# Performance work log

Measured on AMD Instinct MI355X. Metric: run time of the kernel, lower is better.

## Reference

```python
import jax, jax.numpy as jnp
import numpy as np

NUM_HEADS = 12
DIM = 768
HEAD_DIM = DIM // NUM_HEADS


def setup_inputs() -> dict:
    key = jax.random.key(0)
    k1, k2, k3, k4 = jax.random.split(key, 4)
    B, N, C = 4, 8192, DIM
    x = jax.random.normal(k1, (B, N, C), dtype=jnp.float32)
    # torch nn.Linear stores weight as (out_features, in_features)
    W_qkv = jax.random.normal(k2, (3 * C, C), dtype=jnp.float32) * (1.0 / np.sqrt(C))
    W_proj = jax.random.normal(k3, (C, C), dtype=jnp.float32) * (1.0 / np.sqrt(C))
    b_proj = jax.random.normal(k4, (C,), dtype=jnp.float32) * 0.01
    return {"x": x, "W_qkv": W_qkv, "W_proj": W_proj, "b_proj": b_proj}


def reference(x, W_qkv, W_proj, b_proj):
    B, N, C = x.shape
    H, D = NUM_HEADS, HEAD_DIM
    qkv = x @ W_qkv.T                                  # [B,N,3C]
    qkv = qkv.reshape(B, N, 3, H, D).transpose(2, 0, 3, 1, 4)  # [3,B,H,N,D]
    q, k, v = qkv[0], qkv[1], qkv[2]
    q = jax.nn.elu(q) + 1.0
    k = jax.nn.elu(k) + 1.0
    k_sum = k.sum(axis=-2)                             # [B,H,D]
    kv = jnp.einsum('bhnd,bhne->bhde', k, v)           # [B,H,D,D]
    numerator = jnp.einsum('bhnd,bhde->bhne', q, kv)   # [B,H,N,D]
    denominator = jnp.einsum('bhnd,bhd->bhn', q, k_sum)
    out = numerator / (denominator[..., None] + 1e-6)
    out = out.transpose(0, 2, 1, 3).reshape(B, N, C)   # [B,N,C]
    out = out @ W_proj.T + b_proj
    return out
```

## Files before the change

kernel.cpp:

```cpp
#include <hip/hip_runtime.h>
#include <hip/hip_bf16.h>
#include <stdint.h>

typedef __attribute__((ext_vector_type(8))) short short8;
typedef __attribute__((ext_vector_type(4))) float floatx4;

#define NB 4
#define NN 8192
#define NC 768
#define NH 12
#define ND 64
#define LDQKV 2304
#define NSPLIT 16

__device__ __forceinline__ float bf2f(ushort u) {
    union { float f; uint32_t i; } x; x.i = ((uint32_t)u) << 16; return x.f;
}
__device__ __forceinline__ ushort f2bf(float f) {
    union { float f; uint32_t i; } x; x.f = f;
    uint32_t r = x.i + 0x7fff + ((x.i >> 16) & 1);
    return (ushort)(r >> 16);
}
typedef const __attribute__((address_space(1))) uint32_t* gas1_t;
typedef __attribute__((address_space(3))) uint32_t* las3_t;
__device__ __forceinline__ void gl_lds16(const void* g, const void* l) {
    __builtin_amdgcn_global_load_lds((gas1_t)(uintptr_t)g,
                                     (las3_t)(uint32_t)(uintptr_t)l, 16, 0, 0);
}

__global__ __launch_bounds__(256) void cvt_all(const float* __restrict__ X,
                                               const float* __restrict__ Wq,
                                               const float* __restrict__ Wp,
                                               ushort* __restrict__ xbf,
                                               ushort* __restrict__ wqbf,
                                               ushort* __restrict__ wpbf) {
    const int nx = 32768 * 768, nwq = 2304 * 768, nwp = 768 * 768;
    int i = (blockIdx.x * 256 + threadIdx.x) * 8;
    const float* src; ushort* dst;
    if (i < nx)            { src = X + i;              dst = xbf + i; }
    else if (i < nx + nwq) { i -= nx;  src = Wq + i;   dst = wqbf + i; }
    else                   { i -= nx + nwq; if (i >= nwp) return; src = Wp + i; dst = wpbf + i; }
    const float4 a = *(const float4*)src;
    const float4 b = *(const float4*)(src + 4);
    short8 v;
    v[0] = (short)f2bf(a.x); v[1] = (short)f2bf(a.y);
    v[2] = (short)f2bf(a.z); v[3] = (short)f2bf(a.w);
    v[4] = (short)f2bf(b.x); v[5] = (short)f2bf(b.y);
    v[6] = (short)f2bf(b.z); v[7] = (short)f2bf(b.w);
    *(short8*)dst = v;
}

template<int LDC, bool ELU, bool BIAS, typename OutT>
__global__ __launch_bounds__(256) void gemm_bt(const ushort* __restrict__ A,
                                               const ushort* __restrict__ Bw,
                                               const float* __restrict__ bias,
                                               OutT* __restrict__ Cout, int K) {
    __shared__ ushort As[2][128 * 32];
    __shared__ ushort Bs[2][128 * 32];
    const int t = threadIdx.x;
    const int w = t >> 6, lane = t & 63, l16 = lane & 15, quad = lane >> 4;
    const int wm = w & 1, wn = w >> 1;
    const int m0 = blockIdx.y * 128, n0 = blockIdx.x * 128;

    floatx4 acc[4][4] = {};

    const int rowA = t >> 2, chA = t & 3;
    const ushort* gA = A  + (size_t)(m0 + rowA) * K + chA * 8;
    const ushort* gB = Bw + (size_t)(n0 + rowA) * K + chA * 8;

    for (int k0 = 0; k0 < K; k0 += 64) {
        #pragma unroll
        for (int p = 0; p < 2; p++) {
            gl_lds16(gA + k0 + p * 32,                &As[p][w * 512]);
            gl_lds16(gA + k0 + p * 32 + 64 * (size_t)K, &As[p][2048 + w * 512]);
            gl_lds16(gB + k0 + p * 32,                &Bs[p][w * 512]);
            gl_lds16(gB + k0 + p * 32 + 64 * (size_t)K, &Bs[p][2048 + w * 512]);
        }
        __syncthreads();
        #pragma unroll
        for (int p = 0; p < 2; p++) {
            short8 af[4], bfr[4];
            #pragma unroll
            for (int i = 0; i < 4; i++)
                af[i] = *(const short8*)&As[p][(wm * 64 + i * 16 + l16) * 32 + quad * 8];
            #pragma unroll
            for (int j = 0; j < 4; j++)
                bfr[j] = *(const short8*)&Bs[p][(wn * 64 + j * 16 + l16) * 32 + quad * 8];
            #pragma unroll
            for (int i = 0; i < 4; i++)
                #pragma unroll
                for (int j = 0; j < 4; j++)
                    acc[i][j] = __builtin_amdgcn_mfma_f32_16x16x32_bf16(af[i], bfr[j], acc[i][j], 0, 0, 0);
        }
        __syncthreads();
    }

    #pragma unroll
    for (int i = 0; i < 4; i++) {
        const int row = m0 + wm * 64 + i * 16 + quad * 4;
        #pragma unroll
        for (int j = 0; j < 4; j++) {
            const int col = n0 + wn * 64 + j * 16 + l16;
            float bval = 0.f;
            if (BIAS) bval = bias[col];
            OutT* cp = Cout + (size_t)row * LDC + col;
            #pragma unroll
            for (int r = 0; r < 4; r++) {
                float v = acc[i][j][r];
                if (ELU) { if (col < 2 * NC) v = (v > 0.f) ? v + 1.f : __expf(v); }
                if (BIAS) v += bval;
                if (sizeof(OutT) == 2) *cp = (OutT)f2bf(v);
                else                   *cp = (OutT)v;
                cp += LDC;
            }
        }
    }
}

__global__ __launch_bounds__(256) void kv_ksum(const ushort* __restrict__ qkv,
                                               float* __restrict__ kvpart,
                                               float* __restrict__ kspart) {
    __shared__ ushort klds[128 * 64];
    __shared__ ushort vlds[128 * 64];
    __shared__ float  kvred[64 * 64];
    __shared__ float  ksred[4][64];
    const int bh = blockIdx.y, b = bh / NH, h = bh % NH;
    const int t = threadIdx.x, w = t >> 6, lane = t & 63, l16 = lane & 15, quad = lane >> 4;
    const int n0 = blockIdx.x * (NN * NB / NSPLIT / 4);
    const ushort* kbase = qkv + (size_t)(b * NN) * LDQKV + NC     + h * ND;
    const ushort* vbase = qkv + (size_t)(b * NN) * LDQKV + 2 * NC + h * ND;

    floatx4 acc[4][4] = {};
    floatx4 acc5[4] = {};
    short8 ones;
    #pragma unroll
    for (int j = 0; j < 8; j++) ones[j] = (l16 == 0) ? (short)0x3F80 : (short)0;

    const int rowT = t >> 3, ch = t & 7;

    for (int s = 0; s < 4; s++) {
        const int nb = n0 + s * 128;
        #pragma unroll
        for (int i = 0; i < 4; i++) {
            const size_t r = (size_t)(nb + i * 32 + rowT) * LDQKV + ch * 8;
            gl_lds16(kbase + r, klds + i * 2048 + w * 512);
            gl_lds16(vbase + r, vlds + i * 2048 + w * 512);
        }
        __syncthreads();
        short8 af[4], bfr[4];
        #pragma unroll
        for (int dt = 0; dt < 4; dt++) {
            short8 v;
            #pragma unroll
            for (int j = 0; j < 8; j++)
                v[j] = (short)klds[(w * 32 + quad * 8 + j) * 64 + dt * 16 + l16];
            af[dt] = v;
        }
        #pragma unroll
        for (int et = 0; et < 4; et++) {
            short8 v;
            #pragma unroll
            for (int j = 0; j < 8; j++)
                v[j] = (short)vlds[(w * 32 + quad * 8 + j) * 64 + et * 16 + l16];
            bfr[et] = v;
        }
        #pragma unroll
        for (int dt = 0; dt < 4; dt++) {
            #pragma unroll
            for (int et = 0; et < 4; et++)
                acc[dt][et] = __builtin_amdgcn_mfma_f32_16x16x32_bf16(af[dt], bfr[et], acc[dt][et], 0, 0, 0);
            acc5[dt] = __builtin_amdgcn_mfma_f32_16x16x32_bf16(af[dt], ones, acc5[dt], 0, 0, 0);
        }
        __syncthreads();
    }

    if (w == 0) {
        #pragma unroll
        for (int dt = 0; dt < 4; dt++)
            #pragma unroll
            for (int et = 0; et < 4; et++)
                #pragma unroll
                for (int r = 0; r < 4; r++)
                    kvred[(dt * 16 + quad * 4 + r) * 64 + et * 16 + l16] = acc[dt][et][r];
    }
    if (l16 == 0) {
        #pragma unroll
        for (int dt = 0; dt < 4; dt++)
            #pragma unroll
            for (int r = 0; r < 4; r++)
                ksred[w][dt * 16 + quad * 4 + r] = acc5[dt][r];
    }
    __syncthreads();
    if (w != 0) {
        #pragma unroll
        for (int dt = 0; dt < 4; dt++)
            #pragma unroll
            for (int et = 0; et < 4; et++)
                #pragma unroll
                for (int r = 0; r < 4; r++)
                    atomicAdd(&kvred[(dt * 16 + quad * 4 + r) * 64 + et * 16 + l16], acc[dt][et][r]);
    }
    __syncthreads();
    float* kvp = kvpart + ((size_t)blockIdx.x * 48 + bh) * 4096;
    for (int i = t; i < 4096; i += 256) kvp[i] = kvred[i];
    if (t < 64) kspart[((size_t)blockIdx.x * 48 + bh) * 64 + t] =
        ksred[0][t] + ksred[1][t] + ksred[2][t] + ksred[3][t];
}

__global__ __launch_bounds__(256) void reduce_kvks(const float* __restrict__ kvpart,
                                                   const float* __restrict__ kspart,
                                                   float* __restrict__ kvfinal,
                                                   float* __restrict__ ksfinal) {
    const int bh = blockIdx.y, t = threadIdx.x;
    if (blockIdx.x < 16) {
        const int i = blockIdx.x * 256 + t;
        float s = 0.f;
        #pragma unroll
        for (int p = 0; p < NSPLIT; p++) s += kvpart[((size_t)p * 48 + bh) * 4096 + i];
        kvfinal[(size_t)bh * 4096 + i] = s;
    } else if (t < 64) {
        float s = 0.f;
        #pragma unroll
        for (int p = 0; p < NSPLIT; p++) s += kspart[((size_t)p * 48 + bh) * 64 + t];
        ksfinal[bh * 64 + t] = s;
    }
}

__global__ __launch_bounds__(256) void attn_apply(const ushort* __restrict__ qkv,
                                                  const float* __restrict__ kvfinal,
                                                  const float* __restrict__ ksfinal,
                                                  ushort* __restrict__ outpre) {
    __shared__ ushort kvb[64 * 80];
    const int bh = blockIdx.y, b = bh / NH, h = bh % NH;
    const int t = threadIdx.x, w = t >> 6, lane = t & 63, l16 = lane & 15, quad = lane >> 4;

    for (int i = t; i < 4096; i += 256) {
        const int d = i >> 6, e = i & 63;
        kvb[d * 80 + e] = f2bf(kvfinal[(size_t)bh * 4096 + i]);
    }
    for (int i = t; i < 1024; i += 256) {
        const int d = i >> 4, c = i & 15;
        kvb[d * 80 + 64 + c] = (c == 0) ? f2bf(ksfinal[bh * 64 + d]) : (ushort)0;
    }
    __syncthreads();

    short8 bfr[5][2];
    #pragma unroll
    for (int et = 0; et < 5; et++)
        #pragma unroll
        for (int ks = 0; ks < 2; ks++) {
            short8 v;
            #pragma unroll
            for (int j = 0; j < 8; j++)
                v[j] = (short)kvb[(ks * 32 + quad * 8 + j) * 80 + et * 16 + l16];
            bfr[et][ks] = v;
        }

    const ushort* qbase = qkv + (size_t)(b * NN) * LDQKV + h * ND;
    ushort* obase = outpre + (size_t)(b * NN) * NC + h * ND;
    const int n0 = blockIdx.x * (NN * NB / NSPLIT / 4);

    for (int it = 0; it < 8; it++) {
        const int nt = n0 + (it * 4 + w) * 16;
        const ushort* qp = qbase + (size_t)(nt + l16) * LDQKV + quad * 8;
        const short8 a0 = *(const short8*)qp;
        const short8 a1 = *(const short8*)(qp + 32);
        floatx4 acc[5] = {};
        #pragma unroll
        for (int et = 0; et < 5; et++) {
            acc[et] = __builtin_amdgcn_mfma_f32_16x16x32_bf16(a0, bfr[et][0], acc[et], 0, 0, 0);
            acc[et] = __builtin_amdgcn_mfma_f32_16x16x32_bf16(a1, bfr[et][1], acc[et], 0, 0, 0);
        }
        float dv[4];
        #pragma unroll
        for (int r = 0; r < 4; r++) dv[r] = __shfl(acc[4][r], lane & 48);
        #pragma unroll
        for (int et = 0; et < 4; et++)
            #pragma unroll
            for (int r = 0; r < 4; r++) {
                const float o = acc[et][r] / (dv[r] + 1e-6f);
                obase[(size_t)(nt + quad * 4 + r) * NC + et * 16 + l16] = f2bf(o);
            }
    }
}

extern "C" void kernel_launch(void* const* d_in, const int* in_sizes, int n_in,
                              void* d_out, int out_size, void* d_ws, size_t ws_size,
                              hipStream_t stream) {
    (void)in_sizes; (void)n_in; (void)out_size; (void)ws_size;
    const float* X     = (const float*)d_in[0];
    const float* Wqkv  = (const float*)d_in[1];
    const float* Wproj = (const float*)d_in[2];
    const float* bproj = (const float*)d_in[3];
    float* out = (float*)d_out;

    char* ws = (char*)d_ws;
    size_t off = 0;
    ushort* qkv     = (ushort*)(ws + off); off += (size_t)32768 * 2304 * 2;
    ushort* outpre  = (ushort*)(ws + off); off += (size_t)32768 * 768 * 2;
    ushort* xbf     = (ushort*)(ws + off); off += (size_t)32768 * 768 * 2;
    ushort* wqkvbf  = (ushort*)(ws + off); off += (size_t)2304 * 768 * 2;
    ushort* wprojbf = (ushort*)(ws + off); off += (size_t)768 * 768 * 2;
    float* kvpart  = (float*)xbf;
    float* kspart  = kvpart + (size_t)NSPLIT * 48 * 4096;
    float* kvfinal = kspart + (size_t)NSPLIT * 48 * 64;
    float* ksfinal = kvfinal + (size_t)48 * 4096;

    const int ncvt = (32768 * 768 + 2304 * 768 + 768 * 768) / 8 / 256;
    cvt_all<<<ncvt, 256, 0, stream>>>(X, Wqkv, Wproj, xbf, wqkvbf, wprojbf);

    gemm_bt<LDQKV, true, false, ushort><<<dim3(18, 256), 256, 0, stream>>>(xbf, wqkvbf, nullptr, qkv, NC);
    kv_ksum<<<dim3(NSPLIT, 48), 256, 0, stream>>>(qkv, kvpart, kspart);
    reduce_kvks<<<dim3(17, 48), 256, 0, stream>>>(kvpart, kspart, kvfinal, ksfinal);
    attn_apply<<<dim3(NSPLIT, 48), 256, 0, stream>>>(qkv, kvfinal, ksfinal, outpre);
    gemm_bt<NC, false, true, float><<<dim3(6, 256), 256, 0, stream>>>(outpre, wprojbf, bproj, out, NC);
}
```

Measured before the change: 515.0 us.

## Switch GEMM to 32x32x16 MFMA with XOR-swizzled LDS and K=32 steps

The GEMM kernel now uses 32x32x16 bf16 MFMA instructions with 2x2 accumulator tiles per wave in place of 4x4 tiles of 16x16x32. The LDS layout is XOR-swizzled by row to avoid bank conflicts on fragment reads, and the K loop steps by 32 with a single LDS stage instead of two 32-wide stages per iteration. This raises MFMA efficiency and cuts LDS conflicts, but it doubles the number of barrier-synchronised iterations and leaves load latency without overlap. The kv kernels replace an equivalent expression with the constant 512.

```diff
diff --git a/kernel.cpp b/kernel.cpp
--- a/kernel.cpp
+++ b/kernel.cpp
@@ -4,6 +4,7 @@
 
 typedef __attribute__((ext_vector_type(8))) short short8;
 typedef __attribute__((ext_vector_type(4))) float floatx4;
+typedef __attribute__((ext_vector_type(16))) float floatx16;
 
 #define NB 4
 #define NN 8192
@@ -55,66 +56,70 @@
                                                const ushort* __restrict__ Bw,
                                                const float* __restrict__ bias,
                                                OutT* __restrict__ Cout, int K) {
-    __shared__ ushort As[2][128 * 32];
-    __shared__ ushort Bs[2][128 * 32];
+    __shared__ ushort As[128 * 32];
+    __shared__ ushort Bs[128 * 32];
     const int t = threadIdx.x;
-    const int w = t >> 6, lane = t & 63, l16 = lane & 15, quad = lane >> 4;
+    const int w = t >> 6, lane = t & 63, l32 = lane & 31, hi = lane >> 5;
     const int wm = w & 1, wn = w >> 1;
     const int m0 = blockIdx.y * 128, n0 = blockIdx.x * 128;
 
-    floatx4 acc[4][4] = {};
-
-    const int rowA = t >> 2, chA = t & 3;
+    floatx16 acc[2][2] = {};
+
+    const int rowA = t >> 2, chA = (t & 3) ^ (rowA & 3);
     const ushort* gA = A  + (size_t)(m0 + rowA) * K + chA * 8;
     const ushort* gB = Bw + (size_t)(n0 + rowA) * K + chA * 8;
 
-    for (int k0 = 0; k0 < K; k0 += 64) {
-        #pragma unroll
-        for (int p = 0; p < 2; p++) {
-            gl_lds16(gA + k0 + p * 32,                &As[p][w * 512]);
-            gl_lds16(gA + k0 + p * 32 + 64 * (size_t)K, &As[p][2048 + w * 512]);
-            gl_lds16(gB + k0 + p * 32,                &Bs[p][w * 512]);
-            gl_lds16(gB + k0 + p * 32 + 64 * (size_t)K, &Bs[p][2048 + w * 512]);
-        }
+    for (int k0 = 0; k0 < K; k0 += 32) {
+        gl_lds16(gA + k0,                  As + w * 512);
+        gl_lds16(gA + k0 + 64 * (size_t)K, As + 2048 + w * 512);
+        gl_lds16(gB + k0,                  Bs + w * 512);
+        gl_lds16(gB + k0 + 64 * (size_t)K, Bs + 2048 + w * 512);
         __syncthreads();
-        #pragma unroll
-        for (int p = 0; p < 2; p++) {
-            short8 af[4], bfr[4];
-            #pragma unroll
-            for (int i = 0; i < 4; i++)
-                af[i] = *(const short8*)&As[p][(wm * 64 + i * 16 + l16) * 32 + quad * 8];
-            #pragma unroll
-            for (int j = 0; j < 4; j++)
-                bfr[j] = *(const short8*)&Bs[p][(wn * 64 + j * 16 + l16) * 32 + quad * 8];
-            #pragma unroll
-            for (int i = 0; i < 4; i++)
+        short8 af[2][2], bfr[2][2];
+        #pragma unroll
+        for (int mt = 0; mt < 2; mt++)
+            #pragma unroll
+            for (int kh = 0; kh < 2; kh++) {
+                const int row = wm * 64 + mt * 32 + l32;
+                const int kc = kh * 2 + hi;
+                af[mt][kh] = *(const short8*)&As[(row * 4 + (kc ^ (row & 3))) * 8];
+            }
+        #pragma unroll
+        for (int nt = 0; nt < 2; nt++)
+            #pragma unroll
+            for (int kh = 0; kh < 2; kh++) {
+                const int row = wn * 64 + nt * 32 + l32;
+                const int kc = kh * 2 + hi;
+                bfr[nt][kh] = *(const short8*)&Bs[(row * 4 + (kc ^ (row & 3))) * 8];
+            }
+        #pragma unroll
+        for (int mt = 0; mt < 2; mt++)
+            #pragma unroll
+            for (int nt = 0; nt < 2; nt++)
                 #pragma unroll
-                for (int j = 0; j < 4; j++)
-                    acc[i][j] = __builtin_amdgcn_mfma_f32_16x16x32_bf16(af[i], bfr[j], acc[i][j], 0, 0, 0);
-        }
+                for (int kh = 0; kh < 2; kh++)
+                    acc[mt][nt] = __builtin_amdgcn_mfma_f32_32x32x16_bf16(
+                        af[mt][kh], bfr[nt][kh], acc[mt][nt], 0, 0, 0);
         __syncthreads();
     }
 
     #pragma unroll
-    for (int i = 0; i < 4; i++) {
-        const int row = m0 + wm * 64 + i * 16 + quad * 4;
-        #pragma unroll
-        for (int j = 0; j < 4; j++) {
-            const int col = n0 + wn * 64 + j * 16 + l16;
+    for (int mt = 0; mt < 2; mt++)
+        #pragma unroll
+        for (int nt = 0; nt < 2; nt++) {
+            const int col = n0 + wn * 64 + nt * 32 + l32;
             float bval = 0.f;
             if (BIAS) bval = bias[col];
-            OutT* cp = Cout + (size_t)row * LDC + col;
-            #pragma unroll
-            for (int r = 0; r < 4; r++) {
-                float v = acc[i][j][r];
+            #pragma unroll
+            for (int reg = 0; reg < 16; reg++) {
+                const int row = m0 + wm * 64 + mt * 32 + (reg & 3) + 8 * (reg >> 2) + 4 * hi;
+                float v = acc[mt][nt][reg];
                 if (ELU) { if (col < 2 * NC) v = (v > 0.f) ? v + 1.f : __expf(v); }
                 if (BIAS) v += bval;
-                if (sizeof(OutT) == 2) *cp = (OutT)f2bf(v);
-                else                   *cp = (OutT)v;
-                cp += LDC;
+                if (sizeof(OutT) == 2) Cout[(size_t)row * LDC + col] = (OutT)f2bf(v);
+                else                   Cout[(size_t)row * LDC + col] = (OutT)v;
             }
         }
-    }
 }
 
 __global__ __launch_bounds__(256) void kv_ksum(const ushort* __restrict__ qkv,
@@ -126,7 +131,7 @@
     __shared__ float  ksred[4][64];
     const int bh = blockIdx.y, b = bh / NH, h = bh % NH;
     const int t = threadIdx.x, w = t >> 6, lane = t & 63, l16 = lane & 15, quad = lane >> 4;
-    const int n0 = blockIdx.x * (NN * NB / NSPLIT / 4);
+    const int n0 = blockIdx.x * 512;
     const ushort* kbase = qkv + (size_t)(b * NN) * LDQKV + NC     + h * ND;
     const ushort* vbase = qkv + (size_t)(b * NN) * LDQKV + 2 * NC + h * ND;
 
@@ -258,7 +263,7 @@
 
     const ushort* qbase = qkv + (size_t)(b * NN) * LDQKV + h * ND;
     ushort* obase = outpre + (size_t)(b * NN) * NC + h * ND;
-    const int n0 = blockIdx.x * (NN * NB / NSPLIT / 4);
+    const int n0 = blockIdx.x * 512;
 
     for (int it = 0; it < 8; it++) {
         const int nt = n0 + (it * 4 + w) * 16;
```

Result: faster. 503.5 us (-2.2%).

## Shrink GEMM tile to 128x64 with XOR-swizzled LDS and higher occupancy

Applied to the files above, without the earlier changes.

The shared GEMM kernel now uses a 128x64 output tile with a K-step of 32 instead of 128x128 with K-step 64. It XOR-swizzles the 16-byte chunks in LDS to avoid bank conflicts and sets launch bounds to 5 blocks per CU, so more waves are resident to hide latency. The grids double to match. The trade-off is lower arithmetic intensity per tile, more global reloads of A, and twice as many barrier-synchronised K iterations.

```diff
diff --git a/kernel.cpp b/kernel.cpp
--- a/kernel.cpp
+++ b/kernel.cpp
@@ -51,47 +51,46 @@
 }
 
 template<int LDC, bool ELU, bool BIAS, typename OutT>
-__global__ __launch_bounds__(256) void gemm_bt(const ushort* __restrict__ A,
-                                               const ushort* __restrict__ Bw,
-                                               const float* __restrict__ bias,
-                                               OutT* __restrict__ Cout, int K) {
-    __shared__ ushort As[2][128 * 32];
-    __shared__ ushort Bs[2][128 * 32];
+__global__ __launch_bounds__(256, 5) void gemm_bt(const ushort* __restrict__ A,
+                                                  const ushort* __restrict__ Bw,
+                                                  const float* __restrict__ bias,
+                                                  OutT* __restrict__ Cout, int K) {
+    __shared__ ushort As[128 * 32];
+    __shared__ ushort Bs[64 * 32];
     const int t = threadIdx.x;
     const int w = t >> 6, lane = t & 63, l16 = lane & 15, quad = lane >> 4;
     const int wm = w & 1, wn = w >> 1;
-    const int m0 = blockIdx.y * 128, n0 = blockIdx.x * 128;
-
-    floatx4 acc[4][4] = {};
-
-    const int rowA = t >> 2, chA = t & 3;
-    const ushort* gA = A  + (size_t)(m0 + rowA) * K + chA * 8;
-    const ushort* gB = Bw + (size_t)(n0 + rowA) * K + chA * 8;
-
-    for (int k0 = 0; k0 < K; k0 += 64) {
-        #pragma unroll
-        for (int p = 0; p < 2; p++) {
-            gl_lds16(gA + k0 + p * 32,                &As[p][w * 512]);
-            gl_lds16(gA + k0 + p * 32 + 64 * (size_t)K, &As[p][2048 + w * 512]);
-            gl_lds16(gB + k0 + p * 32,                &Bs[p][w * 512]);
-            gl_lds16(gB + k0 + p * 32 + 64 * (size_t)K, &Bs[p][2048 + w * 512]);
-        }
+    const int m0 = blockIdx.y * 128, n0 = blockIdx.x * 64;
+
+    floatx4 acc[4][2] = {};
+
+    const int rT = lane >> 2;
+    const int c4 = (lane & 3) ^ (rT & 3);
+    const ushort* gA1 = A  + (size_t)(m0 + 32 * w + rT) * K + c4 * 8;
+    const ushort* gA2 = gA1 + (size_t)16 * K;
+    const ushort* gB  = Bw + (size_t)(n0 + 16 * w + rT) * K + c4 * 8;
+
+    for (int k0 = 0; k0 < K; k0 += 32) {
+        gl_lds16(gA1 + k0, As + 1024 * w);
+        gl_lds16(gA2 + k0, As + 1024 * w + 512);
+        gl_lds16(gB  + k0, Bs + 512 * w);
         __syncthreads();
-        #pragma unroll
-        for (int p = 0; p < 2; p++) {
-            short8 af[4], bfr[4];
-            #pragma unroll
-            for (int i = 0; i < 4; i++)
-                af[i] = *(const short8*)&As[p][(wm * 64 + i * 16 + l16) * 32 + quad * 8];
-            #pragma unroll
-            for (int j = 0; j < 4; j++)
-                bfr[j] = *(const short8*)&Bs[p][(wn * 64 + j * 16 + l16) * 32 + quad * 8];
-            #pragma unroll
-            for (int i = 0; i < 4; i++)
-                #pragma unroll
-                for (int j = 0; j < 4; j++)
-                    acc[i][j] = __builtin_amdgcn_mfma_f32_16x16x32_bf16(af[i], bfr[j], acc[i][j], 0, 0, 0);
-        }
+        short8 af[4], bfr[2];
+        #pragma unroll
+        for (int i = 0; i < 4; i++) {
+            const int row = wm * 64 + i * 16 + l16;
+            af[i] = *(const short8*)&As[(row * 4 + (quad ^ (l16 & 3))) * 8];
+        }
+        #pragma unroll
+        for (int j = 0; j < 2; j++) {
+            const int row = wn * 32 + j * 16 + l16;
+            bfr[j] = *(const short8*)&Bs[(row * 4 + (quad ^ (l16 & 3))) * 8];
+        }
+        #pragma unroll
+        for (int i = 0; i < 4; i++)
+            #pragma unroll
+            for (int j = 0; j < 2; j++)
+                acc[i][j] = __builtin_amdgcn_mfma_f32_16x16x32_bf16(af[i], bfr[j], acc[i][j], 0, 0, 0);
         __syncthreads();
     }
 
@@ -99,8 +98,8 @@
     for (int i = 0; i < 4; i++) {
         const int row = m0 + wm * 64 + i * 16 + quad * 4;
         #pragma unroll
-        for (int j = 0; j < 4; j++) {
-            const int col = n0 + wn * 64 + j * 16 + l16;
+        for (int j = 0; j < 2; j++) {
+            const int col = n0 + wn * 32 + j * 16 + l16;
             float bval = 0.f;
             if (BIAS) bval = bias[col];
             OutT* cp = Cout + (size_t)row * LDC + col;
@@ -126,7 +125,7 @@
     __shared__ float  ksred[4][64];
     const int bh = blockIdx.y, b = bh / NH, h = bh % NH;
     const int t = threadIdx.x, w = t >> 6, lane = t & 63, l16 = lane & 15, quad = lane >> 4;
-    const int n0 = blockIdx.x * (NN * NB / NSPLIT / 4);
+    const int n0 = blockIdx.x * 512;
     const ushort* kbase = qkv + (size_t)(b * NN) * LDQKV + NC     + h * ND;
     const ushort* vbase = qkv + (size_t)(b * NN) * LDQKV + 2 * NC + h * ND;
 
@@ -258,7 +257,7 @@
 
     const ushort* qbase = qkv + (size_t)(b * NN) * LDQKV + h * ND;
     ushort* obase = outpre + (size_t)(b * NN) * NC + h * ND;
-    const int n0 = blockIdx.x * (NN * NB / NSPLIT / 4);
+    const int n0 = blockIdx.x * 512;
 
     for (int it = 0; it < 8; it++) {
         const int nt = n0 + (it * 4 + w) * 16;
@@ -309,9 +308,9 @@
     const int ncvt = (32768 * 768 + 2304 * 768 + 768 * 768) / 8 / 256;
     cvt_all<<<ncvt, 256, 0, stream>>>(X, Wqkv, Wproj, xbf, wqkvbf, wprojbf);
 
-    gemm_bt<LDQKV, true, false, ushort><<<dim3(18, 256), 256, 0, stream>>>(xbf, wqkvbf, nullptr, qkv, NC);
+    gemm_bt<LDQKV, true, false, ushort><<<dim3(36, 256), 256, 0, stream>>>(xbf, wqkvbf, nullptr, qkv, NC);
     kv_ksum<<<dim3(NSPLIT, 48), 256, 0, stream>>>(qkv, kvpart, kspart);
     reduce_kvks<<<dim3(17, 48), 256, 0, stream>>>(kvpart, kspart, kvfinal, ksfinal);
     attn_apply<<<dim3(NSPLIT, 48), 256, 0, stream>>>(qkv, kvfinal, ksfinal, outpre);
-    gemm_bt<NC, false, true, float><<<dim3(6, 256), 256, 0, stream>>>(outpre, wprojbf, bproj, out, NC);
-}
+    gemm_bt<NC, false, true, float><<<dim3(12, 256), 256, 0, stream>>>(outpre, wprojbf, bproj, out, NC);
+}
```

Measured after the change: 541.4 us. +5.1%, slower.
